# Kernel optimization log

Measured on AMD Instinct MI355X. Metric: run time of the kernel, lower is better.

Reference implementation:

```python
import jax, jax.numpy as jnp
import numpy as np

# --- CQT configuration derived from the layer's __init__ defaults ---
SR = 44100
N_OCTAVES = 7
BINS_PER_SEMITONE = 3
BPO = BINS_PER_SEMITONE * 12            # 36 bins per octave
N_BINS = BPO * N_OCTAVES                # 252 bins
HOP = (int(SR * 11 / 1000.0) // 4) * 4  # 485 -> 484 (hop - hop % 4)
FMIN = 32.70319566257483                # librosa default fmin = C1
Q = 1.0 / (2.0 ** (1.0 / BPO) - 1.0)    # constant-Q factor, filter_scale=1

_FREQS = FMIN * 2.0 ** (np.arange(N_BINS) / BPO)   # [252] center freqs
_LENGTHS = Q * SR / _FREQS                         # per-bin window lengths
MAX_LEN = int(np.ceil(_LENGTHS[0]))                # longest kernel (lowest bin)
CENTER = MAX_LEN // 2
SIG_LEN = 220500                                   # 5 s of audio
N_FRAMES = 1 + SIG_LEN // HOP                      # 456 (centered framing)


def _cqt_kernels():
    """Complex CQT kernel bank, returned as (real, imag) of shape [N_BINS, MAX_LEN].
    Each bin uses a Hann window of its own constant-Q length, centered in MAX_LEN,
    modulated at its center frequency; L1-normalized window and 1/sqrt(L) scaling
    (matching librosa's norm=1 filters with scale=True)."""
    t = jnp.arange(MAX_LEN, dtype=jnp.float32) - CENTER          # centered time axis
    freqs = jnp.asarray(_FREQS, dtype=jnp.float32)[:, None]      # [252, 1]
    L = jnp.asarray(_LENGTHS, dtype=jnp.float32)[:, None]        # [252, 1]
    two_pi = 2.0 * np.pi
    # Hann window of length L_i centered at t=0, zero outside |t| < L_i/2
    win = jnp.where(jnp.abs(t)[None, :] < L / 2,
                    0.5 * (1.0 + jnp.cos(two_pi * t[None, :] / L)),
                    0.0)
    ang = two_pi * freqs * t[None, :] / SR
    norm = win.sum(axis=-1, keepdims=True) * jnp.sqrt(L)
    kr = win * jnp.cos(ang) / norm
    ki = win * jnp.sin(ang) / norm
    return kr, ki


def setup_inputs() -> dict:
    key = jax.random.key(0)
    signal = jax.random.normal(key, (SIG_LEN,), dtype=jnp.float32)
    return {"signal": signal}


def reference(signal) -> jnp.ndarray:
    kr, ki = _cqt_kernels()                                      # [252, MAX_LEN] each
    padded = jnp.pad(signal, (CENTER, CENTER))                   # center=True framing
    idx = (jnp.arange(N_FRAMES)[:, None] * HOP
           + jnp.arange(MAX_LEN)[None, :])                       # [456, MAX_LEN]
    frames = padded[idx]                                         # [456, MAX_LEN]
    cr = frames @ kr.T                                           # [456, 252] real part
    ci = frames @ ki.T                                           # [456, 252] imag part
    mag = jnp.sqrt(cr * cr + ci * ci)                            # |CQT|
    return mag.T                                                 # [252, 456] = (n_bins, n_frames)
```

## Files before the change

kernel.cpp:

```cpp
#include <hip/hip_runtime.h>
#include <hip/hip_bf16.h>
#include <math.h>

#define NBINS    252
#define NFRAMES  456
#define HOPSZ    484
#define SIGLEN   220500
#define TSTART0  (-34688)
#define SRD      44100.0
#define FMIND    32.70319566257483
#define MAXCH    264
#define ASPAN    31520

typedef unsigned short ushort_t;
typedef __attribute__((ext_vector_type(8))) short bf16x8;
typedef __attribute__((ext_vector_type(4))) float f32x4;

struct ChunkTab { int2 e[MAXCH]; };
struct GroupC {
  float fosg[16];
  float invLg[16];
  float ratio[16];
  ushort_t Tfu[256];
};
struct FinC { float nrm[256]; int2 gt[16]; };

__device__ __forceinline__ ushort_t f2bf(float x) {
  __hip_bfloat16 h = __float2bfloat16(x);
  return *reinterpret_cast<ushort_t*>(&h);
}

__device__ __forceinline__ void gen_phase(ushort_t* __restrict__ buf, int sc,
                                          int tbase, int gks, int glane, int gj0,
                                          float fos, float invL, float Tf) {
  const int t0 = tbase + (sc * 4 + gks) * 32 + (glane >> 4) * 8 + gj0;
  ushort_t pr[4], pi[4];
#pragma unroll
  for (int j = 0; j < 4; ++j) {
    const float tt = (float)(t0 + j);
    float kr = 0.0f, ki = 0.0f;
    if (fabsf(tt) <= Tf) {
      float wv = 0.5f + 0.5f * __cosf(6.2831853f * (tt * invL));
      float r = fos * tt; r -= rintf(r);
      float sn, cs; __sincosf(6.2831853f * r, &sn, &cs);
      kr = wv * cs; ki = wv * sn;
    }
    pr[j] = f2bf(kr); pi[j] = f2bf(ki);
  }
  *reinterpret_cast<uint2*>(&buf[gks * 1024 + glane * 8 + gj0])       = *reinterpret_cast<uint2*>(pr);
  *reinterpret_cast<uint2*>(&buf[gks * 1024 + 512 + glane * 8 + gj0]) = *reinterpret_cast<uint2*>(pi);
}

__global__ __launch_bounds__(512) void cqt_fused(const float* __restrict__ sig,
                                                 float* __restrict__ partial,
                                                 ChunkTab tab, GroupC gc) {
  __shared__ ushort_t Alds[ASPAN];
  __shared__ ushort_t Blds[2][4096];

  const int tid = threadIdx.x;
  const int c = blockIdx.y, ft8 = blockIdx.x;
  const int g = tab.e[c].x, jrel = tab.e[c].y;
  const int f0 = ft8 * 64;
  const int S0 = f0 * HOPSZ + TSTART0 + jrel;

  for (int rr = 0; rr < 16; ++rr) {
    const int i = (rr * 512 + tid) * 4;
    if (i < ASPAN) {
      const int s = S0 + i;
      float x0, x1, x2, x3;
      if (s >= 0 && s + 3 < SIGLEN) {
        const float4 v = *reinterpret_cast<const float4*>(sig + s);
        x0 = v.x; x1 = v.y; x2 = v.z; x3 = v.w;
      } else {
        x0 = (s + 0 >= 0 && s + 0 < SIGLEN) ? sig[s + 0] : 0.0f;
        x1 = (s + 1 >= 0 && s + 1 < SIGLEN) ? sig[s + 1] : 0.0f;
        x2 = (s + 2 >= 0 && s + 2 < SIGLEN) ? sig[s + 2] : 0.0f;
        x3 = (s + 3 >= 0 && s + 3 < SIGLEN) ? sig[s + 3] : 0.0f;
      }
      ushort_t* d = &Alds[i];
      d[0] = f2bf(x0); d[1] = f2bf(x1); d[2] = f2bf(x2); d[3] = f2bf(x3);
    }
  }

  const int glane = tid & 63;
  const int gks = (tid >> 6) & 3;
  const int gj0 = (tid >> 8) * 4;
  const int gbl = glane & 15;
  const float fos  = gc.fosg[g]  * gc.ratio[gbl];
  const float invL = gc.invLg[g] * gc.ratio[gbl];
  const float Tf   = (float)gc.Tfu[g * 16 + gbl];
  const int tbase = TSTART0 + jrel;

  const int lane = tid & 63;
  const int w = tid >> 6;
  const int fq = w & 3, ri = w >> 2;
  const int bl = lane & 15, kb = lane >> 4;
  const ushort_t* Ab = &Alds[(fq * 16 + bl) * HOPSZ + kb * 8];

  f32x4 acc = {0.f, 0.f, 0.f, 0.f};

  gen_phase(Blds[0], 0, tbase, gks, glane, gj0, fos, invL, Tf);
  __syncthreads();

  for (int sc = 0; sc < 8; ++sc) {
    if (sc < 7)
      gen_phase(Blds[(sc + 1) & 1], sc + 1, tbase, gks, glane, gj0, fos, invL, Tf);
    const ushort_t* Bb = &Blds[sc & 1][ri * 512 + lane * 8];
#pragma unroll
    for (int k4 = 0; k4 < 4; ++k4) {
      const int ks = sc * 4 + k4;
      union { uint2 q[2]; bf16x8 v; } a;
      a.q[0] = *reinterpret_cast<const uint2*>(Ab + ks * 32);
      a.q[1] = *reinterpret_cast<const uint2*>(Ab + ks * 32 + 4);
      union { uint4 q; bf16x8 v; } b;
      b.q = *reinterpret_cast<const uint4*>(Bb + k4 * 1024);
      acc = __builtin_amdgcn_mfma_f32_16x16x32_bf16(a.v, b.v, acc, 0, 0, 0);
    }
    __syncthreads();
  }

  float* pp = partial + (size_t)(((c * 8 + ft8) * 2 + ri) * 1024 + fq * 256 + bl);
#pragma unroll
  for (int r = 0; r < 4; ++r)
    pp[(kb * 4 + r) * 16] = acc[r];
}

__global__ __launch_bounds__(256) void fin_kernel(const float* __restrict__ partial,
                                                  float* __restrict__ out, FinC fc) {
  const int g = blockIdx.x, ft8 = blockIdx.y;
  const int t = threadIdx.x;
  const int c0 = fc.gt[g].x, nc = fc.gt[g].y;

  float cr[4] = {0.f, 0.f, 0.f, 0.f}, ci[4] = {0.f, 0.f, 0.f, 0.f};
  for (int c = c0; c < c0 + nc; ++c) {
    const float4 vr = *reinterpret_cast<const float4*>(
        partial + (size_t)((c * 8 + ft8) * 2 + 0) * 1024 + t * 4);
    const float4 vi = *reinterpret_cast<const float4*>(
        partial + (size_t)((c * 8 + ft8) * 2 + 1) * 1024 + t * 4);
    cr[0] += vr.x; cr[1] += vr.y; cr[2] += vr.z; cr[3] += vr.w;
    ci[0] += vi.x; ci[1] += vi.y; ci[2] += vi.z; ci[3] += vi.w;
  }
#pragma unroll
  for (int i = 0; i < 4; ++i) {
    const int j = t * 4 + i;
    const int f = ft8 * 64 + (j >> 4);
    const int b = g * 16 + (j & 15);
    if (f < NFRAMES && b < NBINS)
      out[(size_t)b * NFRAMES + f] = fc.nrm[b] * sqrtf(cr[i] * cr[i] + ci[i] * ci[i]);
  }
}

extern "C" void kernel_launch(void* const* d_in, const int* in_sizes, int n_in,
                              void* d_out, int out_size, void* d_ws, size_t ws_size,
                              hipStream_t stream) {
  const float* sig = (const float*)d_in[0];
  float* out = (float*)d_out;

  ChunkTab ctab; GroupC gc; FinC fc;
  const double PI = 3.14159265358979323846;
  const double Q = 1.0 / (exp2(1.0 / 36.0) - 1.0);
  int nch = 0;
  for (int g = 0; g < 16; ++g) {
    double freq = FMIND * exp2((double)(16 * g) / 36.0);
    double L = Q * SRD / freq;
    int T = (int)(L * 0.5);
    int r = (8 - (T & 7)) & 7;
    int tstart = -(T + r);
    int ntaps = 2 * T + 1 + r;
    int chunks = (ntaps + 1023) / 1024;
    gc.fosg[g] = (float)(freq / SRD);
    gc.invLg[g] = (float)(1.0 / L);
    fc.gt[g].x = nch; fc.gt[g].y = chunks;
    int jrel0 = tstart - TSTART0;
    for (int k = 0; k < chunks; ++k) {
      ctab.e[nch].x = g; ctab.e[nch].y = jrel0 + k * 1024; ++nch;
    }
  }
  for (int i = nch; i < MAXCH; ++i) { ctab.e[i].x = 0; ctab.e[i].y = 0; }
  for (int bl = 0; bl < 16; ++bl) gc.ratio[bl] = (float)exp2((double)bl / 36.0);
  for (int b = 0; b < 256; ++b) {
    if (b < NBINS) {
      double freq = FMIND * exp2((double)b / 36.0);
      double L = Q * SRD / freq;
      int T = (int)(L * 0.5);
      double N = (double)(2 * T + 1);
      double win_sum = 0.5 * N - 0.5 * (sin(PI * (N - L) / L) / sin(PI / L));
      gc.Tfu[b] = (ushort_t)T;
      fc.nrm[b] = (float)(1.0 / (win_sum * sqrt(L)));
    } else {
      gc.Tfu[b] = 0; fc.nrm[b] = 0.0f;
    }
  }

  float* partial = (float*)d_ws;

  cqt_fused<<<dim3(8, nch), 512, 0, stream>>>(sig, partial, ctab, gc);
  fin_kernel<<<dim3(16, 8), 256, 0, stream>>>(partial, out, fc);
}
```

Before: 132.1 us.

## Pre-convert padded signal to bf16 and double frame tile per block

```diff
diff --git a/kernel.cpp b/kernel.cpp
--- a/kernel.cpp
+++ b/kernel.cpp
@@ -10,7 +10,10 @@
 #define SRD      44100.0
 #define FMIND    32.70319566257483
 #define MAXCH    264
-#define ASPAN    31520
+#define FT       128
+#define NFT      4
+#define PADBF    321536
+#define AELEMS   65536
 
 typedef unsigned short ushort_t;
 typedef __attribute__((ext_vector_type(8))) short bf16x8;
@@ -30,13 +33,23 @@
   return *reinterpret_cast<ushort_t*>(&h);
 }
 
+__global__ __launch_bounds__(256) void prep_kernel(const float* __restrict__ sig,
+                                                   ushort_t* __restrict__ padbf) {
+  int i = blockIdx.x * 256 + threadIdx.x;
+  if (i < PADBF) {
+    int s = i + TSTART0;
+    float v = (s >= 0 && s < SIGLEN) ? sig[s] : 0.0f;
+    padbf[i] = f2bf(v);
+  }
+}
+
 __device__ __forceinline__ void gen_phase(ushort_t* __restrict__ buf, int sc,
                                           int tbase, int gks, int glane, int gj0,
                                           float fos, float invL, float Tf) {
   const int t0 = tbase + (sc * 4 + gks) * 32 + (glane >> 4) * 8 + gj0;
-  ushort_t pr[4], pi[4];
-#pragma unroll
-  for (int j = 0; j < 4; ++j) {
+  ushort_t pr[2], pi[2];
+#pragma unroll
+  for (int j = 0; j < 2; ++j) {
     const float tt = (float)(t0 + j);
     float kr = 0.0f, ki = 0.0f;
     if (fabsf(tt) <= Tf) {
@@ -47,64 +60,51 @@
     }
     pr[j] = f2bf(kr); pi[j] = f2bf(ki);
   }
-  *reinterpret_cast<uint2*>(&buf[gks * 1024 + glane * 8 + gj0])       = *reinterpret_cast<uint2*>(pr);
-  *reinterpret_cast<uint2*>(&buf[gks * 1024 + 512 + glane * 8 + gj0]) = *reinterpret_cast<uint2*>(pi);
-}
-
-__global__ __launch_bounds__(512) void cqt_fused(const float* __restrict__ sig,
-                                                 float* __restrict__ partial,
-                                                 ChunkTab tab, GroupC gc) {
-  __shared__ ushort_t Alds[ASPAN];
+  *reinterpret_cast<unsigned int*>(&buf[gks * 1024 + glane * 8 + gj0])       = *reinterpret_cast<unsigned int*>(pr);
+  *reinterpret_cast<unsigned int*>(&buf[gks * 1024 + 512 + glane * 8 + gj0]) = *reinterpret_cast<unsigned int*>(pi);
+}
+
+__global__ __launch_bounds__(1024) void cqt_fused(const ushort_t* __restrict__ padbf,
+                                                  float* __restrict__ partial,
+                                                  ChunkTab tab, GroupC gc) {
+  __shared__ ushort_t Alds[AELEMS];
   __shared__ ushort_t Blds[2][4096];
 
   const int tid = threadIdx.x;
-  const int c = blockIdx.y, ft8 = blockIdx.x;
+  const int lane = tid & 63;
+  const int w = tid >> 6;
+  const int c = blockIdx.y, ft = blockIdx.x;
   const int g = tab.e[c].x, jrel = tab.e[c].y;
-  const int f0 = ft8 * 64;
-  const int S0 = f0 * HOPSZ + TSTART0 + jrel;
-
-  for (int rr = 0; rr < 16; ++rr) {
-    const int i = (rr * 512 + tid) * 4;
-    if (i < ASPAN) {
-      const int s = S0 + i;
-      float x0, x1, x2, x3;
-      if (s >= 0 && s + 3 < SIGLEN) {
-        const float4 v = *reinterpret_cast<const float4*>(sig + s);
-        x0 = v.x; x1 = v.y; x2 = v.z; x3 = v.w;
-      } else {
-        x0 = (s + 0 >= 0 && s + 0 < SIGLEN) ? sig[s + 0] : 0.0f;
-        x1 = (s + 1 >= 0 && s + 1 < SIGLEN) ? sig[s + 1] : 0.0f;
-        x2 = (s + 2 >= 0 && s + 2 < SIGLEN) ? sig[s + 2] : 0.0f;
-        x3 = (s + 3 >= 0 && s + 3 < SIGLEN) ? sig[s + 3] : 0.0f;
-      }
-      ushort_t* d = &Alds[i];
-      d[0] = f2bf(x0); d[1] = f2bf(x1); d[2] = f2bf(x2); d[3] = f2bf(x3);
-    }
-  }
-
-  const int glane = tid & 63;
+  const int P0 = ft * FT * HOPSZ + jrel;
+
+  {
+    const uint4* gs = reinterpret_cast<const uint4*>(padbf + P0) + tid;
+    uint4* ls = reinterpret_cast<uint4*>(Alds) + tid;
+#pragma unroll
+    for (int q = 0; q < 8; ++q)
+      ls[q * 1024] = gs[q * 1024];
+  }
+
   const int gks = (tid >> 6) & 3;
-  const int gj0 = (tid >> 8) * 4;
-  const int gbl = glane & 15;
+  const int gj0 = (tid >> 8) * 2;
+  const int gbl = lane & 15;
   const float fos  = gc.fosg[g]  * gc.ratio[gbl];
   const float invL = gc.invLg[g] * gc.ratio[gbl];
   const float Tf   = (float)gc.Tfu[g * 16 + gbl];
   const int tbase = TSTART0 + jrel;
 
-  const int lane = tid & 63;
-  const int w = tid >> 6;
-  const int fq = w & 3, ri = w >> 2;
+  const int fq8 = w >> 1, ri = w & 1;
   const int bl = lane & 15, kb = lane >> 4;
-  const ushort_t* Ab = &Alds[(fq * 16 + bl) * HOPSZ + kb * 8];
+  const ushort_t* Ab = &Alds[(fq8 * 16 + bl) * HOPSZ + kb * 8];
 
   f32x4 acc = {0.f, 0.f, 0.f, 0.f};
 
-  gen_phase(Blds[0], 0, tbase, gks, glane, gj0, fos, invL, Tf);
+  gen_phase(Blds[0], 0, tbase, gks, lane, gj0, fos, invL, Tf);
   __syncthreads();
 
   for (int sc = 0; sc < 8; ++sc) {
     if (sc < 7)
-      gen_phase(Blds[(sc + 1) & 1], sc + 1, tbase, gks, glane, gj0, fos, invL, Tf);
+      gen_phase(Blds[(sc + 1) & 1], sc + 1, tbase, gks, lane, gj0, fos, invL, Tf);
     const ushort_t* Bb = &Blds[sc & 1][ri * 512 + lane * 8];
 #pragma unroll
     for (int k4 = 0; k4 < 4; ++k4) {
@@ -119,31 +119,31 @@
     __syncthreads();
   }
 
-  float* pp = partial + (size_t)(((c * 8 + ft8) * 2 + ri) * 1024 + fq * 256 + bl);
+  float* pp = partial + (size_t)(((c * NFT + ft) * 2 + ri) * 2048 + fq8 * 256 + bl);
 #pragma unroll
   for (int r = 0; r < 4; ++r)
     pp[(kb * 4 + r) * 16] = acc[r];
 }
 
-__global__ __launch_bounds__(256) void fin_kernel(const float* __restrict__ partial,
+__global__ __launch_bounds__(512) void fin_kernel(const float* __restrict__ partial,
                                                   float* __restrict__ out, FinC fc) {
-  const int g = blockIdx.x, ft8 = blockIdx.y;
+  const int g = blockIdx.x, ft = blockIdx.y;
   const int t = threadIdx.x;
   const int c0 = fc.gt[g].x, nc = fc.gt[g].y;
 
   float cr[4] = {0.f, 0.f, 0.f, 0.f}, ci[4] = {0.f, 0.f, 0.f, 0.f};
   for (int c = c0; c < c0 + nc; ++c) {
     const float4 vr = *reinterpret_cast<const float4*>(
-        partial + (size_t)((c * 8 + ft8) * 2 + 0) * 1024 + t * 4);
+        partial + (size_t)((c * NFT + ft) * 2 + 0) * 2048 + t * 4);
     const float4 vi = *reinterpret_cast<const float4*>(
-        partial + (size_t)((c * 8 + ft8) * 2 + 1) * 1024 + t * 4);
+        partial + (size_t)((c * NFT + ft) * 2 + 1) * 2048 + t * 4);
     cr[0] += vr.x; cr[1] += vr.y; cr[2] += vr.z; cr[3] += vr.w;
     ci[0] += vi.x; ci[1] += vi.y; ci[2] += vi.z; ci[3] += vi.w;
   }
 #pragma unroll
   for (int i = 0; i < 4; ++i) {
     const int j = t * 4 + i;
-    const int f = ft8 * 64 + (j >> 4);
+    const int f = ft * FT + (j >> 4);
     const int b = g * 16 + (j & 15);
     if (f < NFRAMES && b < NBINS)
       out[(size_t)b * NFRAMES + f] = fc.nrm[b] * sqrtf(cr[i] * cr[i] + ci[i] * ci[i]);
@@ -155,6 +155,7 @@
                               hipStream_t stream) {
   const float* sig = (const float*)d_in[0];
   float* out = (float*)d_out;
+  char* ws = (char*)d_ws;
 
   ChunkTab ctab; GroupC gc; FinC fc;
   const double PI = 3.14159265358979323846;
@@ -192,8 +193,11 @@
     }
   }
 
-  float* partial = (float*)d_ws;
-
-  cqt_fused<<<dim3(8, nch), 512, 0, stream>>>(sig, partial, ctab, gc);
-  fin_kernel<<<dim3(16, 8), 256, 0, stream>>>(partial, out, fc);
-}
+  ushort_t* padbf = (ushort_t*)ws;
+  size_t off = ((size_t)PADBF * 2 + 255) & ~(size_t)255;
+  float* partial = (float*)(ws + off);
+
+  prep_kernel<<<(PADBF + 255) / 256, 256, 0, stream>>>(sig, padbf);
+  cqt_fused<<<dim3(NFT, nch), 1024, 0, stream>>>(padbf, partial, ctab, gc);
+  fin_kernel<<<dim3(16, NFT), 512, 0, stream>>>(partial, out, fc);
+}
```

Measured after the change: 122.4 us. 7.4% less time.
